# Kernel optimization log

Measured on AMD Instinct MI355X. Metric: run time of the kernel, lower is better.

The kernel has to match this reference:

```python
import jax, jax.numpy as jnp
import numpy as np

N = 50000       # nodes
E = 1600000     # edges (before self-loops)
NFEAT = 256
NHID = 8        # hidden units per head
HEADS = 8
NCLASS = 16
L1 = 0.5        # damping lambda layer 1
L2 = 0.5        # damping lambda layer 2
SLOPE = 0.2     # LeakyReLU negative slope (PyG GATConv default)


def setup_inputs() -> dict:
    ks = jax.random.split(jax.random.key(0), 16)
    g = lambda k, shape, fan: jax.random.normal(k, shape, jnp.float32) * (1.0 / np.sqrt(fan))
    return {
        "x": jax.random.normal(ks[0], (N, NFEAT), jnp.float32),
        "edge_index": jax.random.randint(ks[1], (2, E), 0, N, jnp.int64),
        # conv1: GATConv(nfeat -> nhid, heads=HEADS, concat=True)
        "W1": g(ks[2], (NFEAT, HEADS * NHID), NFEAT),
        "a1_src": g(ks[3], (HEADS, NHID), NHID),
        "a1_dst": g(ks[4], (HEADS, NHID), NHID),
        "b1": jnp.zeros((HEADS * NHID,), jnp.float32),
        # conv2: GATConv(nhid*heads -> nclass, heads=1, concat=False)
        "W2": g(ks[5], (HEADS * NHID, NCLASS), HEADS * NHID),
        "a2_src": g(ks[6], (1, NCLASS), NCLASS),
        "a2_dst": g(ks[7], (1, NCLASS), NCLASS),
        "b2": jnp.zeros((NCLASS,), jnp.float32),
        # side-branch linear layers
        "fc1_W": g(ks[8], (NFEAT, NHID), NFEAT),
        "fc1_b": jnp.zeros((NHID,), jnp.float32),
        "fc2_W": g(ks[9], (HEADS * NHID, NCLASS), HEADS * NHID),
        "fc2_b": jnp.zeros((NCLASS,), jnp.float32),
    }


def gat_conv(x, W, a_src, a_dst, b, src, dst, heads, outc, concat):
    n = x.shape[0]
    h = (x @ W).reshape(n, heads, outc)                 # [N, H, C]
    alpha_s = jnp.sum(h * a_src, axis=-1)               # [N, H]
    alpha_d = jnp.sum(h * a_dst, axis=-1)               # [N, H]
    e = jax.nn.leaky_relu(alpha_s[src] + alpha_d[dst], SLOPE)  # [Etot, H]
    # segment softmax over incoming edges of each destination node
    m = jax.ops.segment_max(e, dst, num_segments=n)
    m = jax.lax.stop_gradient(m)                        # max-shift is grad-neutral
    ex = jnp.exp(e - m[dst])
    denom = jax.ops.segment_sum(ex, dst, num_segments=n)
    alpha = ex / denom[dst]                             # [Etot, H]
    out = jax.ops.segment_sum(h[src] * alpha[:, :, None], dst, num_segments=n)
    if concat:
        out = out.reshape(n, heads * outc)
    else:
        out = out.mean(axis=1)
    return out + b


def reference(x, edge_index, W1, a1_src, a1_dst, b1, W2, a2_src, a2_dst, b2,
              fc1_W, fc1_b, fc2_W, fc2_b):
    loop = jnp.arange(N, dtype=edge_index.dtype)
    src = jnp.concatenate([edge_index[0], loop])
    dst = jnp.concatenate([edge_index[1], loop])
    # layer 1: GATConv + damped linear side branch
    out1 = gat_conv(x, W1, a1_src, a1_dst, b1, src, dst, HEADS, NHID, True)
    side1 = jnp.tile(x @ fc1_W + fc1_b, (1, HEADS))     # cat of heads copies
    h = jax.nn.elu(out1 - L1 * side1)                   # [N, H*C]
    # layer 2
    out2 = gat_conv(h, W2, a2_src, a2_dst, b2, src, dst, 1, NCLASS, False)
    side2 = h @ fc2_W + fc2_b
    return jax.nn.log_softmax(out2 - L2 * side2, axis=1)
```

## Files before the change

kernel.cpp:

```cpp
#include <hip/hip_runtime.h>
#include <hip/hip_bf16.h>
#include <cstddef>

constexpr int N      = 50000;
constexpr int E      = 1600000;
constexpr int NFEAT  = 256;
constexpr float SLOPE = 0.2f;
constexpr float L1d  = 0.5f;
constexpr float L2d  = 0.5f;

constexpr int BSHIFT = 7;
constexpr int NBUK   = (N + 127) >> BSHIFT;
constexpr int EPB    = 4096;
constexpr int NBLK   = (E + EPB - 1) / EPB;
constexpr int CAP    = 5120;

constexpr size_t al64(size_t x) { return (x + 63) & ~size_t(63); }
constexpr size_t W_OFFS  = 0;
constexpr size_t W_CSR   = W_OFFS  + al64(N + 1);
constexpr size_t W_STAGE = W_CSR   + (size_t)E;
constexpr size_t W_BHIST = W_STAGE + (size_t)E;
constexpr size_t W_TOT   = W_BHIST + al64((size_t)NBLK * NBUK);
constexpr size_t W_BBASE = W_TOT   + al64(NBUK);
constexpr size_t W_H1B   = W_BBASE + al64(NBUK + 1);
constexpr size_t W_S1B   = W_H1B   + (size_t)N * 32;
constexpr size_t W_D1    = W_S1B   + (size_t)N * 4;
constexpr size_t W_SIDE1 = W_D1    + (size_t)N * 8;
constexpr size_t W_HF    = W_SIDE1 + (size_t)N * 8;
constexpr size_t W_H2B   = W_HF    + (size_t)N * 64;
constexpr size_t W_SIDE2 = W_H2B   + (size_t)N * 8;
constexpr size_t W_S2B   = W_SIDE2 + (size_t)N * 16;
constexpr size_t W_D2    = W_S2B   + al64(N / 2);

typedef short bf16x8 __attribute__((ext_vector_type(8)));
typedef float f32x4  __attribute__((ext_vector_type(4)));

__device__ inline short f2bf(float f) {
    unsigned u = __builtin_bit_cast(unsigned, f);
    u += 0x7FFF + ((u >> 16) & 1);
    return (short)(u >> 16);
}

__device__ inline float bfu2f(unsigned short u) {
    return __builtin_bit_cast(float, (unsigned)u << 16);
}

#define SWZ8(x, PAT) __builtin_bit_cast(float, __builtin_amdgcn_ds_swizzle(__builtin_bit_cast(int, (x)), (PAT)))


__global__ __launch_bounds__(256) void p1_hist_kernel(const int* __restrict__ ei,
                                                      int* __restrict__ bhist) {
    __shared__ int hist[NBUK];
    int tid = threadIdx.x;
    for (int j = tid; j < NBUK; j += 256) hist[j] = 0;
    __syncthreads();
    int base = blockIdx.x * EPB;
    int end = base + EPB; if (end > E) end = E;
    for (int i = base + tid; i < end; i += 256) {
        int d = ei[E + i];
        atomicAdd(&hist[d >> BSHIFT], 1);
    }
    __syncthreads();
    for (int j = tid; j < NBUK; j += 256) bhist[(size_t)blockIdx.x * NBUK + j] = hist[j];
}

__global__ __launch_bounds__(512) void s1_scan_kernel(int* __restrict__ bhist,
                                                      int* __restrict__ tot) {
    __shared__ int sd[512];
    int tid = threadIdx.x;
    int b = blockIdx.x;
    int v = (tid < NBLK) ? bhist[(size_t)tid * NBUK + b] : 0;
    sd[tid] = v;
    __syncthreads();
    for (int off = 1; off < 512; off <<= 1) {
        int t = (tid >= off) ? sd[tid - off] : 0;
        __syncthreads();
        sd[tid] += t;
        __syncthreads();
    }
    if (tid < NBLK) bhist[(size_t)tid * NBUK + b] = sd[tid] - v;
    if (tid == 511) tot[b] = sd[511];
}

__global__ __launch_bounds__(512) void s2_scan_kernel(const int* __restrict__ tot,
                                                      int* __restrict__ bbase,
                                                      int* __restrict__ offs) {
    __shared__ int sd[512];
    int tid = threadIdx.x;
    int v = (tid < NBUK) ? tot[tid] : 0;
    sd[tid] = v;
    __syncthreads();
    for (int off = 1; off < 512; off <<= 1) {
        int t = (tid >= off) ? sd[tid - off] : 0;
        __syncthreads();
        sd[tid] += t;
        __syncthreads();
    }
    if (tid < NBUK) bbase[tid] = sd[tid] - v;
    if (tid == 0) { bbase[NBUK] = E; offs[N] = E; }
}

__global__ __launch_bounds__(256) void p2_stage_kernel(const int* __restrict__ ei,
                                                       const int* __restrict__ bhist,
                                                       const int* __restrict__ bbase,
                                                       unsigned int* __restrict__ stage) {
    __shared__ int cur[NBUK];
    int tid = threadIdx.x;
    for (int j = tid; j < NBUK; j += 256)
        cur[j] = bbase[j] + bhist[(size_t)blockIdx.x * NBUK + j];
    __syncthreads();
    int base = blockIdx.x * EPB;
    int end = base + EPB; if (end > E) end = E;
    for (int i = base + tid; i < end; i += 256) {
        int s = ei[i];
        int d = ei[E + i];
        int b = d >> BSHIFT;
        int pos = atomicAdd(&cur[b], 1);
        stage[pos] = ((unsigned int)(d & 127) << 24) | (unsigned int)s;
    }
}

__global__ __launch_bounds__(256) void p3_fine_kernel(const unsigned int* __restrict__ stage,
                                                      const int* __restrict__ bbase,
                                                      int* __restrict__ offs,
                                                      int* __restrict__ csr) {
    __shared__ unsigned int sstage[CAP];
    __shared__ int hist[128];
    __shared__ int scn[128];
    __shared__ int cur[128];
    int tid = threadIdx.x;
    int b = blockIdx.x;
    int ebase = bbase[b], eend = bbase[b + 1];
    int cnt = eend - ebase;
    if (tid < 128) hist[tid] = 0;
    __syncthreads();
    for (int i = tid; i < cnt; i += 256) {
        unsigned int p = stage[ebase + i];
        if (i < CAP) sstage[i] = p;
        atomicAdd(&hist[p >> 24], 1);
    }
    __syncthreads();
    if (tid < 128) scn[tid] = hist[tid];
    __syncthreads();
    for (int off = 1; off < 128; off <<= 1) {
        int t = (tid < 128 && tid >= off) ? scn[tid - off] : 0;
        __syncthreads();
        if (tid < 128) scn[tid] += t;
        __syncthreads();
    }
    if (tid < 128) {
        int excl = scn[tid] - hist[tid];
        cur[tid] = excl;
        int v = (b << BSHIFT) + tid;
        if (v < N) offs[v] = ebase + excl;
    }
    __syncthreads();
    for (int i = tid; i < cnt; i += 256) {
        unsigned int p = (i < CAP) ? sstage[i] : stage[ebase + i];
        int dloc = (int)(p >> 24);
        int s = (int)(p & 0xFFFFFFu);
        int r = atomicAdd(&cur[dloc], 1);
        csr[ebase + r] = s;
    }
}

__global__ __launch_bounds__(256) void gemm1_kernel(const float* __restrict__ x,
                                                    const float* __restrict__ W1,
                                                    const float* __restrict__ fc1W,
                                                    const float* __restrict__ fc1b,
                                                    short* __restrict__ h1b,
                                                    float* __restrict__ side1) {
    __shared__ bf16x8 wfrag[2560];
    int tid = threadIdx.x;

    for (int s = tid; s < 2560; s += 256) {
        int l = s & 63;
        int t = s >> 6;
        int nt = t % 5, kt = t / 5;
        int col = nt * 16 + (l & 15);
        int kbase = kt * 32 + (l >> 4) * 8;
        bf16x8 v;
#pragma unroll
        for (int j = 0; j < 8; ++j) {
            float f = 0.f;
            if (col < 64)      f = W1[(size_t)(kbase + j) * 64 + col];
            else if (col < 72) f = fc1W[(size_t)(kbase + j) * 8 + (col - 64)];
            v[j] = f2bf(f);
        }
        wfrag[s] = v;
    }
    __syncthreads();

    int w = tid >> 6;
    int l = tid & 63;
    int row0 = blockIdx.x * 64;
    int arow = row0 + w * 16 + (l & 15);
    if (arow >= N) arow = N - 1;
    const float* ap = x + (size_t)arow * NFEAT + ((l >> 4) * 8);

    f32x4 acc[5];
#pragma unroll
    for (int nt = 0; nt < 5; ++nt) acc[nt] = (f32x4){0.f, 0.f, 0.f, 0.f};

#pragma unroll
    for (int kt = 0; kt < 8; ++kt) {
        float4 alo = *reinterpret_cast<const float4*>(ap + kt * 32);
        float4 ahi = *reinterpret_cast<const float4*>(ap + kt * 32 + 4);
        bf16x8 af;
        af[0] = f2bf(alo.x); af[1] = f2bf(alo.y); af[2] = f2bf(alo.z); af[3] = f2bf(alo.w);
        af[4] = f2bf(ahi.x); af[5] = f2bf(ahi.y); af[6] = f2bf(ahi.z); af[7] = f2bf(ahi.w);
#pragma unroll
        for (int nt = 0; nt < 5; ++nt) {
            acc[nt] = __builtin_amdgcn_mfma_f32_16x16x32_bf16(
                af, wfrag[(kt * 5 + nt) * 64 + l], acc[nt], 0, 0, 0);
        }
    }

    int cbase = l & 15;
    int rbase = row0 + w * 16 + (l >> 4) * 4;
#pragma unroll
    for (int nt = 0; nt < 4; ++nt) {
#pragma unroll
        for (int r = 0; r < 4; ++r) {
            int row = rbase + r;
            if (row < N) h1b[(size_t)row * 64 + nt * 16 + cbase] = f2bf(acc[nt][r]);
        }
    }
    if (cbase < 8) {
        float bb = fc1b[cbase];
#pragma unroll
        for (int r = 0; r < 4; ++r) {
            int row = rbase + r;
            if (row < N) side1[(size_t)row * 8 + cbase] = acc[4][r] + bb;
        }
    }
}

__global__ __launch_bounds__(256) void alpha1_kernel(const __hip_bfloat16* __restrict__ h1b,
                                                     const float* __restrict__ a1s,
                                                     const float* __restrict__ a1d,
                                                     __hip_bfloat16* __restrict__ s1b,
                                                     float* __restrict__ d1) {
    int wave = threadIdx.x >> 6;
    int lane = threadIdx.x & 63;
    int v = blockIdx.x * 4 + wave;
    if (v >= N) return;
    float hv = __bfloat162float(h1b[(size_t)v * 64 + lane]);
    float sa = hv * a1s[lane];
    float sd = hv * a1d[lane];
#pragma unroll
    for (int off = 1; off < 8; off <<= 1) {
        sa += __shfl_xor(sa, off, 64);
        sd += __shfl_xor(sd, off, 64);
    }
    if ((lane & 7) == 0) {
        s1b[v * 8 + (lane >> 3)] = __float2bfloat16(sa);
        d1[v * 8 + (lane >> 3)] = sd;
    }
}

__global__ __launch_bounds__(256) void agg1_kernel(const int* __restrict__ offs,
                                                   const int* __restrict__ csr,
                                                   const unsigned short* __restrict__ h1u,
                                                   const unsigned short* __restrict__ s1u,
                                                   const float* __restrict__ d1,
                                                   const float* __restrict__ side1,
                                                   const float* __restrict__ b1,
                                                   float* __restrict__ hf) {
    int lane = threadIdx.x & 63;
    int v = blockIdx.x * 4 + (threadIdx.x >> 6);
    if (v >= N) return;
    int j  = lane & 7;
    int hh = lane >> 3;

    float dv = d1[v * 8 + hh];

    float e0 = bfu2f(s1u[v * 8 + hh]) + dv;
    e0 = fmaxf(e0, SLOPE * e0);
    float ex0 = __expf(e0);
    float acc = ex0 * bfu2f(h1u[(size_t)v * 64 + lane]);
    float den0 = ex0;
    float den_att = 0.f;

    int beg = offs[v], end = offs[v + 1];
    int deg = end - beg;
    int ngf = deg >> 3;
    int rem = deg & 7;

    const int* cb = csr + beg;

    unsigned short hA[8], hB[8];
    int s8A = 0, s8B = 0;
    float svA = 0.f, svB = 0.f;

#define LOADH(s8, h)                                                        \
    do {                                                                     \
        int sj0 = __builtin_amdgcn_readlane(s8, 0);                          \
        int sj1 = __builtin_amdgcn_readlane(s8, 1);                          \
        int sj2 = __builtin_amdgcn_readlane(s8, 2);                          \
        int sj3 = __builtin_amdgcn_readlane(s8, 3);                          \
        int sj4 = __builtin_amdgcn_readlane(s8, 4);                          \
        int sj5 = __builtin_amdgcn_readlane(s8, 5);                          \
        int sj6 = __builtin_amdgcn_readlane(s8, 6);                          \
        int sj7 = __builtin_amdgcn_readlane(s8, 7);                          \
        h[0] = h1u[((size_t)sj0 << 6) + lane];                               \
        h[1] = h1u[((size_t)sj1 << 6) + lane];                               \
        h[2] = h1u[((size_t)sj2 << 6) + lane];                               \
        h[3] = h1u[((size_t)sj3 << 6) + lane];                               \
        h[4] = h1u[((size_t)sj4 << 6) + lane];                               \
        h[5] = h1u[((size_t)sj5 << 6) + lane];                               \
        h[6] = h1u[((size_t)sj6 << 6) + lane];                               \
        h[7] = h1u[((size_t)sj7 << 6) + lane];                               \
    } while (0)

#define COMP(sv, h)                                                          \
    do {                                                                     \
        float a = (sv) + dv;                                                 \
        a = fmaxf(a, SLOPE * a);                                             \
        float xv = __expf(a);                                                \
        den_att += xv;                                                       \
        acc += SWZ8(xv, 0x018) * bfu2f(h[0]);                                \
        acc += SWZ8(xv, 0x038) * bfu2f(h[1]);                                \
        acc += SWZ8(xv, 0x058) * bfu2f(h[2]);                                \
        acc += SWZ8(xv, 0x078) * bfu2f(h[3]);                                \
        acc += SWZ8(xv, 0x098) * bfu2f(h[4]);                                \
        acc += SWZ8(xv, 0x0B8) * bfu2f(h[5]);                                \
        acc += SWZ8(xv, 0x0D8) * bfu2f(h[6]);                                \
        acc += SWZ8(xv, 0x0F8) * bfu2f(h[7]);                                \
    } while (0)

    if (ngf > 0) {
        s8A = cb[j];
        svA = bfu2f(s1u[s8A * 8 + hh]);
        LOADH(s8A, hA);
        if (ngf > 1) s8B = cb[8 + j];
    }
    int g = 0;
    for (; g + 1 < ngf; g += 2) {
        svB = bfu2f(s1u[s8B * 8 + hh]);
        LOADH(s8B, hB);
        int s8C = (g + 2 < ngf) ? cb[(g + 2) * 8 + j] : 0;
        COMP(svA, hA);
        s8A = s8C;
        if (g + 2 < ngf) {
            svA = bfu2f(s1u[s8A * 8 + hh]);
            LOADH(s8A, hA);
        }
        int s8D = (g + 3 < ngf) ? cb[(g + 3) * 8 + j] : 0;
        COMP(svB, hB);
        s8B = s8D;
    }
    if (g < ngf) COMP(svA, hA);

    if (rem) {
        int idx = beg + ngf * 8 + j;
        idx = idx < end ? idx : end - 1;
        int s8 = csr[idx];
        float a = bfu2f(s1u[s8 * 8 + hh]) + dv;
        a = fmaxf(a, SLOPE * a);
        float xv = __expf(a);
        xv = (j < rem) ? xv : 0.f;
        den_att += xv;
        unsigned short ht[8];
        LOADH(s8, ht);
        acc += SWZ8(xv, 0x018) * bfu2f(ht[0]);
        acc += SWZ8(xv, 0x038) * bfu2f(ht[1]);
        acc += SWZ8(xv, 0x058) * bfu2f(ht[2]);
        acc += SWZ8(xv, 0x078) * bfu2f(ht[3]);
        acc += SWZ8(xv, 0x098) * bfu2f(ht[4]);
        acc += SWZ8(xv, 0x0B8) * bfu2f(ht[5]);
        acc += SWZ8(xv, 0x0D8) * bfu2f(ht[6]);
        acc += SWZ8(xv, 0x0F8) * bfu2f(ht[7]);
    }
#undef LOADH
#undef COMP

    den_att += __shfl_xor(den_att, 1, 64);
    den_att += __shfl_xor(den_att, 2, 64);
    den_att += __shfl_xor(den_att, 4, 64);
    float den = den0 + den_att;

    float o = acc / den + b1[lane];
    float z = o - L1d * side1[v * 8 + j];
    hf[(size_t)v * 64 + lane] = z > 0.f ? z : (__expf(z) - 1.f);
}

__global__ __launch_bounds__(256) void gemm2_kernel(const float* __restrict__ hf,
                                                    const float* __restrict__ W2,
                                                    const float* __restrict__ fc2W,
                                                    const float* __restrict__ fc2b,
                                                    __hip_bfloat16* __restrict__ h2b,
                                                    float* __restrict__ side2) {
    __shared__ float xs[128][65];
    __shared__ float ws[64][33];
    int tid = threadIdx.x;
    int ty = tid >> 3;
    int tx = tid & 7;
    int row0 = blockIdx.x * 128;

    float acc[4][4];
#pragma unroll
    for (int i = 0; i < 4; ++i)
#pragma unroll
        for (int j = 0; j < 4; ++j) acc[i][j] = 0.f;

    int lr = tid >> 4;
    int lj = tid & 15;
#pragma unroll
    for (int it = 0; it < 8; ++it) {
        int r = lr + it * 16;
        int grow = row0 + r;
        if (grow >= N) grow = N - 1;
        float4 vv = *reinterpret_cast<const float4*>(&hf[(size_t)grow * 64 + lj * 4]);
        xs[r][lj * 4 + 0] = vv.x;
        xs[r][lj * 4 + 1] = vv.y;
        xs[r][lj * 4 + 2] = vv.z;
        xs[r][lj * 4 + 3] = vv.w;
    }
    for (int idx = tid; idx < 64 * 32; idx += 256) {
        int k = idx >> 5;
        int c = idx & 31;
        float v = (c < 16) ? W2[(size_t)k * 16 + c] : fc2W[(size_t)k * 16 + (c - 16)];
        ws[k][c] = v;
    }
    __syncthreads();
#pragma unroll 4
    for (int k = 0; k < 64; ++k) {
        float xv[4], wv[4];
#pragma unroll
        for (int i = 0; i < 4; ++i) xv[i] = xs[ty * 4 + i][k];
#pragma unroll
        for (int j = 0; j < 4; ++j) wv[j] = ws[k][tx * 4 + j];
#pragma unroll
        for (int i = 0; i < 4; ++i)
#pragma unroll
            for (int j = 0; j < 4; ++j) acc[i][j] += xv[i] * wv[j];
    }

#pragma unroll
    for (int i = 0; i < 4; ++i) {
        int row = row0 + ty * 4 + i;
        if (row >= N) continue;
#pragma unroll
        for (int j = 0; j < 4; ++j) {
            int c = tx * 4 + j;
            if (c < 16) h2b[(size_t)row * 16 + c] = __float2bfloat16(acc[i][j]);
            else        side2[(size_t)row * 16 + (c - 16)] = acc[i][j] + fc2b[c - 16];
        }
    }
}

__global__ __launch_bounds__(256) void alpha2_kernel(const __hip_bfloat16* __restrict__ h2b,
                                                     const float* __restrict__ a2s,
                                                     const float* __restrict__ a2d,
                                                     __hip_bfloat16* __restrict__ s2b,
                                                     float* __restrict__ d2) {
    int wave = threadIdx.x >> 6;
    int lane = threadIdx.x & 63;
    int vbase = (blockIdx.x * 4 + wave) * 4;
    int r = lane >> 4;
    int c = lane & 15;
    int v = vbase + r;
    float hv = (v < N) ? __bfloat162float(h2b[(size_t)v * 16 + c]) : 0.f;
    float sa = hv * a2s[c];
    float sd = hv * a2d[c];
#pragma unroll
    for (int off = 1; off < 16; off <<= 1) {
        sa += __shfl_xor(sa, off, 64);
        sd += __shfl_xor(sd, off, 64);
    }
    if (v < N && c == 0) {
        s2b[v] = __float2bfloat16(sa);
        d2[v] = sd;
    }
}

__global__ __launch_bounds__(256) void agg2_kernel(const int* __restrict__ offs,
                                                   const int* __restrict__ csr,
                                                   const unsigned short* __restrict__ h2u,
                                                   const unsigned short* __restrict__ s2u,
                                                   const float* __restrict__ d2,
                                                   const float* __restrict__ side2,
                                                   const float* __restrict__ b2,
                                                   float* __restrict__ out) {
    int lane = threadIdx.x & 63;
    int v = blockIdx.x * 4 + (threadIdx.x >> 6);
    if (v >= N) return;
    int c = lane & 15;
    int slot = lane >> 4;
    int j4 = lane & 3;
    int slotaddr = slot << 2;
    float dv = d2[v];

    float acc = 0.f, den = 0.f;
    if (slot == 0) {
        float e = bfu2f(s2u[v]) + dv;
        e = fmaxf(e, SLOPE * e);
        float ex = __expf(e);
        acc = ex * bfu2f(h2u[(size_t)v * 16 + c]);
        den = ex;
    }
    int beg = offs[v], end = offs[v + 1];
    int deg = end - beg;
    int ngf = deg >> 2;
    int rem = deg & 3;
    const int* cb = csr + beg;

#define COMP2(s4, sv)                                                        \
    do {                                                                     \
        float a = (sv) + dv;                                                 \
        a = fmaxf(a, SLOPE * a);                                             \
        float xv = __expf(a);                                                \
        float xs = __builtin_bit_cast(float,                                 \
            __builtin_amdgcn_ds_bpermute(slotaddr, __builtin_bit_cast(int, xv))); \
        int ss = __builtin_amdgcn_ds_bpermute(slotaddr, (s4));               \
        float hv = bfu2f(h2u[((size_t)ss << 4) + c]);                        \
        acc += xs * hv;                                                      \
        den += xs;                                                           \
    } while (0)

    int s4A = 0, s4B = 0;
    float svA = 0.f, svB = 0.f;
    if (ngf > 0) {
        s4A = cb[j4];
        svA = bfu2f(s2u[s4A]);
        if (ngf > 1) s4B = cb[4 + j4];
    }
    int g = 0;
    for (; g + 1 < ngf; g += 2) {
        svB = bfu2f(s2u[s4B]);
        int s4C = (g + 2 < ngf) ? cb[(g + 2) * 4 + j4] : 0;
        COMP2(s4A, svA);
        s4A = s4C;
        if (g + 2 < ngf) svA = bfu2f(s2u[s4A]);
        int s4D = (g + 3 < ngf) ? cb[(g + 3) * 4 + j4] : 0;
        COMP2(s4B, svB);
        s4B = s4D;
    }
    if (g < ngf) COMP2(s4A, svA);

    if (rem) {
        int idx = beg + ngf * 4 + j4;
        idx = idx < end ? idx : end - 1;
        int s4 = csr[idx];
        float a = bfu2f(s2u[s4]) + dv;
        a = fmaxf(a, SLOPE * a);
        float xv = __expf(a);
        xv = (j4 < rem) ? xv : 0.f;
        float xs = __builtin_bit_cast(float,
            __builtin_amdgcn_ds_bpermute(slotaddr, __builtin_bit_cast(int, xv)));
        int ss = __builtin_amdgcn_ds_bpermute(slotaddr, s4);
        float hv = bfu2f(h2u[((size_t)ss << 4) + c]);
        acc += xs * hv;
        den += xs;
    }
#undef COMP2

    acc += __shfl_xor(acc, 16, 64);
    acc += __shfl_xor(acc, 32, 64);
    den += __shfl_xor(den, 16, 64);
    den += __shfl_xor(den, 32, 64);

    float o = acc / den + b2[c];
    float z = o - L2d * side2[(size_t)v * 16 + c];

    float m = z;
#pragma unroll
    for (int off = 1; off < 16; off <<= 1) m = fmaxf(m, __shfl_xor(m, off, 64));
    float ex = __expf(z - m);
    float s = ex;
#pragma unroll
    for (int off = 1; off < 16; off <<= 1) s += __shfl_xor(s, off, 64);
    float lsm = z - m - __logf(s);
    if (slot == 0) out[(size_t)v * 16 + c] = lsm;
}

extern "C" void kernel_launch(void* const* d_in, const int* in_sizes, int n_in,
                              void* d_out, int out_size, void* d_ws, size_t ws_size,
                              hipStream_t stream) {
    const float* x    = (const float*)d_in[0];
    const int*   ei   = (const int*)d_in[1];
    const float* W1   = (const float*)d_in[2];
    const float* a1s  = (const float*)d_in[3];
    const float* a1d  = (const float*)d_in[4];
    const float* b1   = (const float*)d_in[5];
    const float* W2   = (const float*)d_in[6];
    const float* a2s  = (const float*)d_in[7];
    const float* a2d  = (const float*)d_in[8];
    const float* b2   = (const float*)d_in[9];
    const float* fc1W = (const float*)d_in[10];
    const float* fc1b = (const float*)d_in[11];
    const float* fc2W = (const float*)d_in[12];
    const float* fc2b = (const float*)d_in[13];
    float* out = (float*)d_out;

    int*   wsi = (int*)d_ws;
    float* wsf = (float*)d_ws;
    int*   offs   = wsi + W_OFFS;
    int*   csr    = wsi + W_CSR;
    unsigned int* stage = (unsigned int*)(wsi + W_STAGE);
    int*   bhist  = wsi + W_BHIST;
    int*   tot    = wsi + W_TOT;
    int*   bbase  = wsi + W_BBASE;
    __hip_bfloat16* h1b = (__hip_bfloat16*)(wsf + W_H1B);
    __hip_bfloat16* s1b = (__hip_bfloat16*)(wsf + W_S1B);
    float* d1     = wsf + W_D1;
    float* side1  = wsf + W_SIDE1;
    float* hf     = wsf + W_HF;
    __hip_bfloat16* h2b = (__hip_bfloat16*)(wsf + W_H2B);
    float* side2  = wsf + W_SIDE2;
    __hip_bfloat16* s2b = (__hip_bfloat16*)(wsf + W_S2B);
    float* d2     = wsf + W_D2;

    p1_hist_kernel<<<NBLK, 256, 0, stream>>>(ei, bhist);
    s1_scan_kernel<<<NBUK, 512, 0, stream>>>(bhist, tot);
    s2_scan_kernel<<<1, 512, 0, stream>>>(tot, bbase, offs);
    p2_stage_kernel<<<NBLK, 256, 0, stream>>>(ei, bhist, bbase, stage);
    p3_fine_kernel<<<NBUK, 256, 0, stream>>>(stage, bbase, offs, csr);

    gemm1_kernel<<<(N + 63) / 64, 256, 0, stream>>>(x, W1, fc1W, fc1b,
                                                    (short*)h1b, side1);
    alpha1_kernel<<<(N + 3) / 4, 256, 0, stream>>>(h1b, a1s, a1d, s1b, d1);
    agg1_kernel<<<(N + 3) / 4, 256, 0, stream>>>(offs, csr,
                                                 (const unsigned short*)h1b,
                                                 (const unsigned short*)s1b,
                                                 d1, side1, b1, hf);

    gemm2_kernel<<<(N + 127) / 128, 256, 0, stream>>>(hf, W2, fc2W, fc2b, h2b, side2);
    alpha2_kernel<<<(N + 15) / 16, 256, 0, stream>>>(h2b, a2s, a2d, s2b, d2);
    agg2_kernel<<<(N + 3) / 4, 256, 0, stream>>>(offs, csr,
                                                 (const unsigned short*)h2b,
                                                 (const unsigned short*)s2b,
                                                 d2, side2, b2, out);
}
```

Before: 171.0 us.

## Precompute per-edge attention exponentials in separate kernels before aggregation

Adds att1/att2 kernels that walk the bucketed CSR (which now keeps the destination-local index in the top byte) and write each edge's exp(leaky_relu(s+d)) as bf16 into new edge-ordered buffers. Self-loop weights are computed in the alpha kernels. The aggregation kernels then read these precomputed weights instead of gathering s[src], computing exp and shuffling via swizzle/bpermute, which shortens their critical path. The cost is two extra launches plus writing and re-reading about E*8 and E bf16 values, with exp weights rounded to bf16.

New measurement: 256.3 us. 1.5x slower.

```diff
diff --git a/kernel.cpp b/kernel.cpp
--- a/kernel.cpp
+++ b/kernel.cpp
@@ -31,6 +31,10 @@
 constexpr size_t W_SIDE2 = W_H2B   + (size_t)N * 8;
 constexpr size_t W_S2B   = W_SIDE2 + (size_t)N * 16;
 constexpr size_t W_D2    = W_S2B   + al64(N / 2);
+constexpr size_t W_XA1   = W_D2    + al64(N);
+constexpr size_t W_XS1   = W_XA1   + (size_t)E * 4 + 64;
+constexpr size_t W_XA2   = W_XS1   + (size_t)N * 4;
+constexpr size_t W_XS2   = W_XA2   + (size_t)E / 2 + 64;
 
 typedef short bf16x8 __attribute__((ext_vector_type(8)));
 typedef float f32x4  __attribute__((ext_vector_type(4)));
@@ -44,8 +48,6 @@
 __device__ inline float bfu2f(unsigned short u) {
     return __builtin_bit_cast(float, (unsigned)u << 16);
 }
-
-#define SWZ8(x, PAT) __builtin_bit_cast(float, __builtin_amdgcn_ds_swizzle(__builtin_bit_cast(int, (x)), (PAT)))
 
 
 __global__ __launch_bounds__(256) void p1_hist_kernel(const int* __restrict__ ei,
@@ -123,7 +125,7 @@
 __global__ __launch_bounds__(256) void p3_fine_kernel(const unsigned int* __restrict__ stage,
                                                       const int* __restrict__ bbase,
                                                       int* __restrict__ offs,
-                                                      int* __restrict__ csr) {
+                                                      unsigned int* __restrict__ csr) {
     __shared__ unsigned int sstage[CAP];
     __shared__ int hist[128];
     __shared__ int scn[128];
@@ -158,9 +160,8 @@
     for (int i = tid; i < cnt; i += 256) {
         unsigned int p = (i < CAP) ? sstage[i] : stage[ebase + i];
         int dloc = (int)(p >> 24);
-        int s = (int)(p & 0xFFFFFFu);
         int r = atomicAdd(&cur[dloc], 1);
-        csr[ebase + r] = s;
+        csr[ebase + r] = p;
     }
 }
 
@@ -240,7 +241,8 @@
                                                      const float* __restrict__ a1s,
                                                      const float* __restrict__ a1d,
                                                      __hip_bfloat16* __restrict__ s1b,
-                                                     float* __restrict__ d1) {
+                                                     float* __restrict__ d1,
+                                                     unsigned short* __restrict__ xs1) {
     int wave = threadIdx.x >> 6;
     int lane = threadIdx.x & 63;
     int v = blockIdx.x * 4 + wave;
@@ -256,44 +258,67 @@
     if ((lane & 7) == 0) {
         s1b[v * 8 + (lane >> 3)] = __float2bfloat16(sa);
         d1[v * 8 + (lane >> 3)] = sd;
-    }
-}
-
-__global__ __launch_bounds__(256) void agg1_kernel(const int* __restrict__ offs,
-                                                   const int* __restrict__ csr,
-                                                   const unsigned short* __restrict__ h1u,
+        float e = sa + sd;
+        e = fmaxf(e, SLOPE * e);
+        xs1[v * 8 + (lane >> 3)] = (unsigned short)f2bf(__expf(e));
+    }
+}
+
+__global__ __launch_bounds__(256) void att1_kernel(const unsigned int* __restrict__ csr,
+                                                   const int* __restrict__ bbase,
                                                    const unsigned short* __restrict__ s1u,
                                                    const float* __restrict__ d1,
+                                                   unsigned short* __restrict__ xa1) {
+    int b = blockIdx.x;
+    int base = bbase[b], cnt = bbase[b + 1] - base;
+    int tid = threadIdx.x;
+    int lane = tid & 63;
+    int w = tid >> 6;
+    int j = lane >> 3, h = lane & 7;
+    int dbase = (b << BSHIFT) * 8;
+    for (int i0 = w * 8; i0 < cnt; i0 += 32) {
+        int i = i0 + j;
+        int ic = i < cnt ? i : cnt - 1;
+        unsigned p = csr[base + ic];
+        int src = (int)(p & 0xFFFFFFu);
+        int dloc = (int)(p >> 24);
+        float sv = bfu2f(s1u[src * 8 + h]);
+        float dvv = d1[dbase + dloc * 8 + h];
+        float a = sv + dvv;
+        a = fmaxf(a, SLOPE * a);
+        float xv = __expf(a);
+        if (i < cnt) xa1[(((size_t)(base + i)) << 3) + h] = (unsigned short)f2bf(xv);
+    }
+}
+
+__global__ __launch_bounds__(256) void agg1_kernel(const int* __restrict__ offs,
+                                                   const unsigned int* __restrict__ csr,
+                                                   const unsigned short* __restrict__ h1u,
+                                                   const unsigned short* __restrict__ xa1,
+                                                   const unsigned short* __restrict__ xs1,
                                                    const float* __restrict__ side1,
                                                    const float* __restrict__ b1,
                                                    float* __restrict__ hf) {
     int lane = threadIdx.x & 63;
     int v = blockIdx.x * 4 + (threadIdx.x >> 6);
     if (v >= N) return;
-    int j  = lane & 7;
-    int hh = lane >> 3;
-
-    float dv = d1[v * 8 + hh];
-
-    float e0 = bfu2f(s1u[v * 8 + hh]) + dv;
-    e0 = fmaxf(e0, SLOPE * e0);
-    float ex0 = __expf(e0);
-    float acc = ex0 * bfu2f(h1u[(size_t)v * 64 + lane]);
-    float den0 = ex0;
-    float den_att = 0.f;
+    int hc = lane >> 3;
+    int j8 = lane & 7;
+
+    float xs = bfu2f(xs1[v * 8 + hc]);
+    float acc = xs * bfu2f(h1u[((size_t)v << 6) + lane]);
+    float den = xs;
 
     int beg = offs[v], end = offs[v + 1];
     int deg = end - beg;
-    int ngf = deg >> 3;
-    int rem = deg & 7;
-
-    const int* cb = csr + beg;
+    int ngf = deg >> 3, rem = deg & 7;
+    const unsigned int* cb = csr + beg;
+    const unsigned short* xq0 = xa1 + ((size_t)beg << 3);
 
     unsigned short hA[8], hB[8];
     int s8A = 0, s8B = 0;
-    float svA = 0.f, svB = 0.f;
-
-#define LOADH(s8, h)                                                        \
+
+#define LOADH1(s8, h)                                                        \
     do {                                                                     \
         int sj0 = __builtin_amdgcn_readlane(s8, 0);                          \
         int sj1 = __builtin_amdgcn_readlane(s8, 1);                          \
@@ -313,76 +338,54 @@
         h[7] = h1u[((size_t)sj7 << 6) + lane];                               \
     } while (0)
 
-#define COMP(sv, h)                                                          \
+#define COMP1(xq, h)                                                         \
     do {                                                                     \
-        float a = (sv) + dv;                                                 \
-        a = fmaxf(a, SLOPE * a);                                             \
-        float xv = __expf(a);                                                \
-        den_att += xv;                                                       \
-        acc += SWZ8(xv, 0x018) * bfu2f(h[0]);                                \
-        acc += SWZ8(xv, 0x038) * bfu2f(h[1]);                                \
-        acc += SWZ8(xv, 0x058) * bfu2f(h[2]);                                \
-        acc += SWZ8(xv, 0x078) * bfu2f(h[3]);                                \
-        acc += SWZ8(xv, 0x098) * bfu2f(h[4]);                                \
-        acc += SWZ8(xv, 0x0B8) * bfu2f(h[5]);                                \
-        acc += SWZ8(xv, 0x0D8) * bfu2f(h[6]);                                \
-        acc += SWZ8(xv, 0x0F8) * bfu2f(h[7]);                                \
+        _Pragma("unroll")                                                    \
+        for (int jj = 0; jj < 8; ++jj) {                                     \
+            float xv = bfu2f((xq)[jj * 8 + hc]);                             \
+            acc += xv * bfu2f(h[jj]);                                        \
+            den += xv;                                                       \
+        }                                                                    \
     } while (0)
 
     if (ngf > 0) {
-        s8A = cb[j];
-        svA = bfu2f(s1u[s8A * 8 + hh]);
-        LOADH(s8A, hA);
-        if (ngf > 1) s8B = cb[8 + j];
+        s8A = (int)(cb[j8] & 0xFFFFFFu);
+        LOADH1(s8A, hA);
+        if (ngf > 1) s8B = (int)(cb[8 + j8] & 0xFFFFFFu);
     }
     int g = 0;
     for (; g + 1 < ngf; g += 2) {
-        svB = bfu2f(s1u[s8B * 8 + hh]);
-        LOADH(s8B, hB);
-        int s8C = (g + 2 < ngf) ? cb[(g + 2) * 8 + j] : 0;
-        COMP(svA, hA);
+        LOADH1(s8B, hB);
+        int s8C = (g + 2 < ngf) ? (int)(cb[(g + 2) * 8 + j8] & 0xFFFFFFu) : 0;
+        COMP1(xq0 + ((size_t)g << 6), hA);
         s8A = s8C;
-        if (g + 2 < ngf) {
-            svA = bfu2f(s1u[s8A * 8 + hh]);
-            LOADH(s8A, hA);
-        }
-        int s8D = (g + 3 < ngf) ? cb[(g + 3) * 8 + j] : 0;
-        COMP(svB, hB);
+        if (g + 2 < ngf) LOADH1(s8A, hA);
+        int s8D = (g + 3 < ngf) ? (int)(cb[(g + 3) * 8 + j8] & 0xFFFFFFu) : 0;
+        COMP1(xq0 + ((size_t)(g + 1) << 6), hB);
         s8B = s8D;
     }
-    if (g < ngf) COMP(svA, hA);
+    if (g < ngf) COMP1(xq0 + ((size_t)g << 6), hA);
 
     if (rem) {
-        int idx = beg + ngf * 8 + j;
+        int idx = beg + ngf * 8 + j8;
         idx = idx < end ? idx : end - 1;
-        int s8 = csr[idx];
-        float a = bfu2f(s1u[s8 * 8 + hh]) + dv;
-        a = fmaxf(a, SLOPE * a);
-        float xv = __expf(a);
-        xv = (j < rem) ? xv : 0.f;
-        den_att += xv;
+        int s8 = (int)(csr[idx] & 0xFFFFFFu);
         unsigned short ht[8];
-        LOADH(s8, ht);
-        acc += SWZ8(xv, 0x018) * bfu2f(ht[0]);
-        acc += SWZ8(xv, 0x038) * bfu2f(ht[1]);
-        acc += SWZ8(xv, 0x058) * bfu2f(ht[2]);
-        acc += SWZ8(xv, 0x078) * bfu2f(ht[3]);
-        acc += SWZ8(xv, 0x098) * bfu2f(ht[4]);
-        acc += SWZ8(xv, 0x0B8) * bfu2f(ht[5]);
-        acc += SWZ8(xv, 0x0D8) * bfu2f(ht[6]);
-        acc += SWZ8(xv, 0x0F8) * bfu2f(ht[7]);
-    }
-#undef LOADH
-#undef COMP
-
-    den_att += __shfl_xor(den_att, 1, 64);
-    den_att += __shfl_xor(den_att, 2, 64);
-    den_att += __shfl_xor(den_att, 4, 64);
-    float den = den0 + den_att;
+        LOADH1(s8, ht);
+        const unsigned short* xq = xq0 + ((size_t)ngf << 6);
+#pragma unroll
+        for (int jj = 0; jj < 8; ++jj) {
+            float xv = (jj < rem) ? bfu2f(xq[jj * 8 + hc]) : 0.f;
+            acc += xv * bfu2f(ht[jj]);
+            den += xv;
+        }
+    }
+#undef LOADH1
+#undef COMP1
 
     float o = acc / den + b1[lane];
-    float z = o - L1d * side1[v * 8 + j];
-    hf[(size_t)v * 64 + lane] = z > 0.f ? z : (__expf(z) - 1.f);
+    float z = o - L1d * side1[v * 8 + j8];
+    hf[((size_t)v << 6) + lane] = z > 0.f ? z : (__expf(z) - 1.f);
 }
 
 __global__ __launch_bounds__(256) void gemm2_kernel(const float* __restrict__ hf,
@@ -454,7 +457,8 @@
                                                      const float* __restrict__ a2s,
                                                      const float* __restrict__ a2d,
                                                      __hip_bfloat16* __restrict__ s2b,
-                                                     float* __restrict__ d2) {
+                                                     float* __restrict__ d2,
+                                                     unsigned short* __restrict__ xs2) {
     int wave = threadIdx.x >> 6;
     int lane = threadIdx.x & 63;
     int vbase = (blockIdx.x * 4 + wave) * 4;
@@ -472,14 +476,35 @@
     if (v < N && c == 0) {
         s2b[v] = __float2bfloat16(sa);
         d2[v] = sd;
-    }
-}
-
-__global__ __launch_bounds__(256) void agg2_kernel(const int* __restrict__ offs,
-                                                   const int* __restrict__ csr,
-                                                   const unsigned short* __restrict__ h2u,
+        float e = sa + sd;
+        e = fmaxf(e, SLOPE * e);
+        xs2[v] = (unsigned short)f2bf(__expf(e));
+    }
+}
+
+__global__ __launch_bounds__(256) void att2_kernel(const unsigned int* __restrict__ csr,
+                                                   const int* __restrict__ bbase,
                                                    const unsigned short* __restrict__ s2u,
                                                    const float* __restrict__ d2,
+                                                   unsigned short* __restrict__ xa2) {
+    int b = blockIdx.x;
+    int base = bbase[b], cnt = bbase[b + 1] - base;
+    int dbase = b << BSHIFT;
+    for (int i = threadIdx.x; i < cnt; i += 256) {
+        unsigned p = csr[base + i];
+        int src = (int)(p & 0xFFFFFFu);
+        int dloc = (int)(p >> 24);
+        float a = bfu2f(s2u[src]) + d2[dbase + dloc];
+        a = fmaxf(a, SLOPE * a);
+        xa2[base + i] = (unsigned short)f2bf(__expf(a));
+    }
+}
+
+__global__ __launch_bounds__(256) void agg2_kernel(const int* __restrict__ offs,
+                                                   const unsigned int* __restrict__ csr,
+                                                   const unsigned short* __restrict__ h2u,
+                                                   const unsigned short* __restrict__ xa2,
+                                                   const unsigned short* __restrict__ xs2,
                                                    const float* __restrict__ side2,
                                                    const float* __restrict__ b2,
                                                    float* __restrict__ out) {
@@ -488,73 +513,64 @@
     if (v >= N) return;
     int c = lane & 15;
     int slot = lane >> 4;
-    int j4 = lane & 3;
-    int slotaddr = slot << 2;
-    float dv = d2[v];
 
     float acc = 0.f, den = 0.f;
     if (slot == 0) {
-        float e = bfu2f(s2u[v]) + dv;
-        e = fmaxf(e, SLOPE * e);
-        float ex = __expf(e);
-        acc = ex * bfu2f(h2u[(size_t)v * 16 + c]);
-        den = ex;
+        float xs = bfu2f(xs2[v]);
+        acc = xs * bfu2f(h2u[(size_t)v * 16 + c]);
+        den = xs;
     }
     int beg = offs[v], end = offs[v + 1];
     int deg = end - beg;
-    int ngf = deg >> 2;
-    int rem = deg & 3;
-    const int* cb = csr + beg;
-
-#define COMP2(s4, sv)                                                        \
-    do {                                                                     \
-        float a = (sv) + dv;                                                 \
-        a = fmaxf(a, SLOPE * a);                                             \
-        float xv = __expf(a);                                                \
-        float xs = __builtin_bit_cast(float,                                 \
-            __builtin_amdgcn_ds_bpermute(slotaddr, __builtin_bit_cast(int, xv))); \
-        int ss = __builtin_amdgcn_ds_bpermute(slotaddr, (s4));               \
-        float hv = bfu2f(h2u[((size_t)ss << 4) + c]);                        \
-        acc += xs * hv;                                                      \
-        den += xs;                                                           \
-    } while (0)
-
-    int s4A = 0, s4B = 0;
-    float svA = 0.f, svB = 0.f;
+    int ngf = deg >> 2, rem = deg & 3;
+
+    int sA = 0, sB = 0;
+    float xA = 0.f, xB = 0.f;
     if (ngf > 0) {
-        s4A = cb[j4];
-        svA = bfu2f(s2u[s4A]);
-        if (ngf > 1) s4B = cb[4 + j4];
+        int i0 = beg + slot;
+        sA = (int)(csr[i0] & 0xFFFFFFu);
+        xA = bfu2f(xa2[i0]);
+        if (ngf > 1) {
+            int i1 = beg + 4 + slot;
+            sB = (int)(csr[i1] & 0xFFFFFFu);
+            xB = bfu2f(xa2[i1]);
+        }
     }
     int g = 0;
     for (; g + 1 < ngf; g += 2) {
-        svB = bfu2f(s2u[s4B]);
-        int s4C = (g + 2 < ngf) ? cb[(g + 2) * 4 + j4] : 0;
-        COMP2(s4A, svA);
-        s4A = s4C;
-        if (g + 2 < ngf) svA = bfu2f(s2u[s4A]);
-        int s4D = (g + 3 < ngf) ? cb[(g + 3) * 4 + j4] : 0;
-        COMP2(s4B, svB);
-        s4B = s4D;
-    }
-    if (g < ngf) COMP2(s4A, svA);
-
+        float x0 = xA;
+        float hv0 = bfu2f(h2u[((size_t)sA << 4) + c]);
+        if (g + 2 < ngf) {
+            int i = beg + (g + 2) * 4 + slot;
+            sA = (int)(csr[i] & 0xFFFFFFu);
+            xA = bfu2f(xa2[i]);
+        }
+        acc += x0 * hv0;
+        den += x0;
+        float x1 = xB;
+        float hv1 = bfu2f(h2u[((size_t)sB << 4) + c]);
+        if (g + 3 < ngf) {
+            int i = beg + (g + 3) * 4 + slot;
+            sB = (int)(csr[i] & 0xFFFFFFu);
+            xB = bfu2f(xa2[i]);
+        }
+        acc += x1 * hv1;
+        den += x1;
+    }
+    if (g < ngf) {
+        float hv = bfu2f(h2u[((size_t)sA << 4) + c]);
+        acc += xA * hv;
+        den += xA;
+    }
     if (rem) {
-        int idx = beg + ngf * 4 + j4;
+        int idx = beg + ngf * 4 + slot;
         idx = idx < end ? idx : end - 1;
-        int s4 = csr[idx];
-        float a = bfu2f(s2u[s4]) + dv;
-        a = fmaxf(a, SLOPE * a);
-        float xv = __expf(a);
-        xv = (j4 < rem) ? xv : 0.f;
-        float xs = __builtin_bit_cast(float,
-            __builtin_amdgcn_ds_bpermute(slotaddr, __builtin_bit_cast(int, xv)));
-        int ss = __builtin_amdgcn_ds_bpermute(slotaddr, s4);
-        float hv = bfu2f(h2u[((size_t)ss << 4) + c]);
-        acc += xs * hv;
-        den += xs;
-    }
-#undef COMP2
+        int s = (int)(csr[idx] & 0xFFFFFFu);
+        float xv = (slot < rem) ? bfu2f(xa2[idx]) : 0.f;
+        float hv = bfu2f(h2u[((size_t)s << 4) + c]);
+        acc += xv * hv;
+        den += xv;
+    }
 
     acc += __shfl_xor(acc, 16, 64);
     acc += __shfl_xor(acc, 32, 64);
@@ -597,7 +613,7 @@
     int*   wsi = (int*)d_ws;
     float* wsf = (float*)d_ws;
     int*   offs   = wsi + W_OFFS;
-    int*   csr    = wsi + W_CSR;
+    unsigned int* csr = (unsigned int*)(wsi + W_CSR);
     unsigned int* stage = (unsigned int*)(wsi + W_STAGE);
     int*   bhist  = wsi + W_BHIST;
     int*   tot    = wsi + W_TOT;
@@ -611,6 +627,10 @@
     float* side2  = wsf + W_SIDE2;
     __hip_bfloat16* s2b = (__hip_bfloat16*)(wsf + W_S2B);
     float* d2     = wsf + W_D2;
+    unsigned short* xa1 = (unsigned short*)(wsf + W_XA1);
+    unsigned short* xs1 = (unsigned short*)(wsf + W_XS1);
+    unsigned short* xa2 = (unsigned short*)(wsf + W_XA2);
+    unsigned short* xs2 = (unsigned short*)(wsf + W_XS2);
 
     p1_hist_kernel<<<NBLK, 256, 0, stream>>>(ei, bhist);
     s1_scan_kernel<<<NBUK, 512, 0, stream>>>(bhist, tot);
@@ -620,16 +640,18 @@
 
     gemm1_kernel<<<(N + 63) / 64, 256, 0, stream>>>(x, W1, fc1W, fc1b,
                                                     (short*)h1b, side1);
-    alpha1_kernel<<<(N + 3) / 4, 256, 0, stream>>>(h1b, a1s, a1d, s1b, d1);
+    alpha1_kernel<<<(N + 3) / 4, 256, 0, stream>>>(h1b, a1s, a1d, s1b, d1, xs1);
+    att1_kernel<<<NBUK, 256, 0, stream>>>(csr, bbase,
+                                          (const unsigned short*)s1b, d1, xa1);
     agg1_kernel<<<(N + 3) / 4, 256, 0, stream>>>(offs, csr,
                                                  (const unsigned short*)h1b,
-                                                 (const unsigned short*)s1b,
-                                                 d1, side1, b1, hf);
+                                                 xa1, xs1, side1, b1, hf);
 
     gemm2_kernel<<<(N + 127) / 128, 256, 0, stream>>>(hf, W2, fc2W, fc2b, h2b, side2);
-    alpha2_kernel<<<(N + 15) / 16, 256, 0, stream>>>(h2b, a2s, a2d, s2b, d2);
+    alpha2_kernel<<<(N + 15) / 16, 256, 0, stream>>>(h2b, a2s, a2d, s2b, d2, xs2);
+    att2_kernel<<<NBUK, 256, 0, stream>>>(csr, bbase,
+                                          (const unsigned short*)s2b, d2, xa2);
     agg2_kernel<<<(N + 3) / 4, 256, 0, stream>>>(offs, csr,
                                                  (const unsigned short*)h2b,
-                                                 (const unsigned short*)s2b,
-                                                 d2, side2, b2, out);
-}
+                                                 xa2, xs2, side2, b2, out);
+}
```
